# Optimization experiments

Measured on AMD Instinct MI355X. Metric: run time of the kernel, lower is better.

## Reference

```python
import jax, jax.numpy as jnp
import numpy as np

H = 12  # max_heads

def setup_inputs() -> dict:
    key = jax.random.key(0)
    ks = jax.random.split(key, 5)
    B, N, E = 8, 1024, 768
    return {
        "x": jax.random.normal(ks[0], (B, N, E), dtype=jnp.float32),
        "w_qkv": jax.random.normal(ks[1], (3 * E, E), dtype=jnp.float32) * 0.02,
        "b_qkv": jax.random.normal(ks[2], (3 * E,), dtype=jnp.float32) * 0.02,
        "w_proj": jax.random.normal(ks[3], (E, E), dtype=jnp.float32) * 0.02,
        "b_proj": jax.random.normal(ks[4], (E,), dtype=jnp.float32) * 0.02,
        "active_heads": 8,
    }

def reference(x, w_qkv, b_qkv, w_proj, b_proj, active_heads):
    B, N, E = x.shape
    D = E // H
    scale = D ** -0.5
    # qkv projection: [B,N,3E] -> [3,B,H,N,D]
    qkv = (x @ w_qkv.T + b_qkv).reshape(B, N, 3, H, D)
    qkv = jnp.transpose(qkv, (2, 0, 3, 1, 4))
    q, k, v = qkv[0], qkv[1], qkv[2]
    # head mask from active_heads (static int)
    head_mask = (jnp.arange(H) < active_heads).astype(x.dtype)
    m = head_mask[None, :, None, None]
    q = q * m
    k = k * m
    v = v * m
    attn = jax.nn.softmax(jnp.einsum("bhqd,bhkd->bhqk", q, k) * scale, axis=-1)
    out = jnp.einsum("bhqk,bhkd->bhqd", attn, v)
    out = jnp.transpose(out, (0, 2, 1, 3)).reshape(B, N, E)
    channel_mask = jnp.repeat(head_mask, D)  # [E]
    out = out * channel_mask[None, None, :]
    return out @ w_proj.T + b_proj
```

## Files before the change

### kernel.cpp

```cpp
#include <hip/hip_runtime.h>
#include <hip/hip_fp16.h>

#define NH 12
#define BSZ 8
#define NSEQ 1024
#define EDIM 768
#define DH 64

typedef _Float16 f16;
typedef f16 half8 __attribute__((ext_vector_type(8)));
typedef f16 half4 __attribute__((ext_vector_type(4)));
typedef float f32x4 __attribute__((ext_vector_type(4)));
typedef unsigned int u32;
typedef u32 u32x2 __attribute__((ext_vector_type(2)));

static __device__ __forceinline__ void gload16(const void* g, void* l) {
    __builtin_amdgcn_global_load_lds((const __attribute__((address_space(1))) u32*)g,
                                     (__attribute__((address_space(3))) u32*)l, 16, 0, 0);
}
static __device__ __forceinline__ u32 pkrtz(float a, float b) {
    auto h = __builtin_amdgcn_cvt_pkrtz(a, b);
    return __builtin_bit_cast(u32, h);
}
#define MFMA16(a, b, c) __builtin_amdgcn_mfma_f32_16x16x32_f16((a), (b), (c), 0, 0, 0)

__global__ void cvt_all_kernel(const float* __restrict__ x, const float* __restrict__ wq,
                               const float* __restrict__ wp, f16* __restrict__ dst) {
    const int NX = BSZ * NSEQ * EDIM;
    const int NWQ = 3 * EDIM * EDIM;
    int i = (blockIdx.x * blockDim.x + threadIdx.x) * 4;
    const float* s;
    int j;
    if (i < NX) { s = x; j = i; }
    else if (i < NX + NWQ) { s = wq; j = i - NX; }
    else { s = wp; j = i - NX - NWQ; }
    float4 v = *(const float4*)(s + j);
    half4 o = { (f16)v.x, (f16)v.y, (f16)v.z, (f16)v.w };
    *(half4*)(dst + i) = o;
}

template<int MODE>
__global__ __launch_bounds__(256) void gemm_kernel(
    const f16* __restrict__ A, const f16* __restrict__ Wt, const float* __restrict__ bias,
    f16* __restrict__ qbuf, f16* __restrict__ kbuf, f16* __restrict__ vbuf,
    float* __restrict__ outp, const int* __restrict__ activep, int Kd, int NCd)
{
    __shared__ __align__(16) f16 Ah[2][2][4][64][8];
    __shared__ __align__(16) f16 Bh[2][2][4][64][8];

    constexpr int K = EDIM;
    constexpr int NKT = K / 32;
    constexpr int NB = (MODE == 0) ? 18 : 6;

    const int lin = blockIdx.x;
    const int xcd = lin & 7, pos = lin >> 3;
    const int bx = pos % NB;
    const int my = xcd + (pos / NB) * 8;
    const int c0 = bx * 128;
    const int m0 = my * 128;
    const int ah = *activep;
    if (MODE == 0) {
        if (((c0 % EDIM) >> 6) >= ah) return;
    }
    const int nkt = (MODE == 1) ? (2 * ah) : NKT;
    const int tid = threadIdx.x;
    const int lane = tid & 63;
    const int wid  = tid >> 6;
    const int wr = wid >> 1;
    const int wc = wid & 1;
    const int r16 = lane & 15, rg = lane >> 4;

    f32x4 acc[4][4];
#pragma unroll
    for (int i = 0; i < 4; ++i)
#pragma unroll
        for (int j = 0; j < 4; ++j)
            acc[i][j] = f32x4{0.f, 0.f, 0.f, 0.f};

    const int s0 = 2 * wid, s1 = 2 * wid + 1;
    const f16* gA0 = A  + (size_t)(m0 + (s0 >> 2) * 64 + (s0 & 3) * 16 + r16) * K + rg * 8;
    const f16* gA1 = A  + (size_t)(m0 + (s1 >> 2) * 64 + (s1 & 3) * 16 + r16) * K + rg * 8;
    const f16* gB0 = Wt + (size_t)(c0 + (s0 >> 2) * 64 + (s0 & 3) * 16 + r16) * K + rg * 8;
    const f16* gB1 = Wt + (size_t)(c0 + (s1 >> 2) * 64 + (s1 & 3) * 16 + r16) * K + rg * 8;

    auto stage = [&](int buf, int kt) {
        gload16(gA0 + kt * 32, &Ah[buf][s0 >> 2][s0 & 3][0][0]);
        gload16(gA1 + kt * 32, &Ah[buf][s1 >> 2][s1 & 3][0][0]);
        gload16(gB0 + kt * 32, &Bh[buf][s0 >> 2][s0 & 3][0][0]);
        gload16(gB1 + kt * 32, &Bh[buf][s1 >> 2][s1 & 3][0][0]);
    };

    if (nkt > 0) stage(0, 0);
    if (nkt > 1) stage(1, 1);
    asm volatile("s_waitcnt vmcnt(4)" ::: "memory");
    __builtin_amdgcn_s_barrier();
    __builtin_amdgcn_sched_barrier(0);

#pragma unroll 1
    for (int kt = 0; kt < nkt; ++kt) {
        const int cur = kt & 1;
        half8 af[4], bf[4];
#pragma unroll
        for (int f = 0; f < 4; ++f) {
            af[f] = *(const half8*)&Ah[cur][wr][f][lane][0];
            bf[f] = *(const half8*)&Bh[cur][wc][f][lane][0];
        }
        asm volatile("s_waitcnt lgkmcnt(0)" ::: "memory");
        __builtin_amdgcn_sched_barrier(0);
        __builtin_amdgcn_s_barrier();
        __builtin_amdgcn_sched_barrier(0);
        if (kt + 2 < nkt) stage(cur, kt + 2);
        __builtin_amdgcn_sched_barrier(0);
        __builtin_amdgcn_s_setprio(1);
#pragma unroll
        for (int fm = 0; fm < 4; ++fm)
#pragma unroll
            for (int fn = 0; fn < 4; ++fn)
                acc[fm][fn] = MFMA16(af[fm], bf[fn], acc[fm][fn]);
        __builtin_amdgcn_s_setprio(0);
        if (kt + 1 < nkt) {
            if (kt + 2 < nkt) asm volatile("s_waitcnt vmcnt(4)" ::: "memory");
            else              asm volatile("s_waitcnt vmcnt(0)" ::: "memory");
            __builtin_amdgcn_s_barrier();
            __builtin_amdgcn_sched_barrier(0);
        }
    }

#pragma unroll
    for (int fn = 0; fn < 4; ++fn) {
        const int c = c0 + wc * 64 + fn * 16 + r16;
        const float bv = bias[c];
        const bool colActive = (MODE == 1) || (((c % EDIM) >> 6) < ah);
#pragma unroll
        for (int fm = 0; fm < 4; ++fm) {
            const int mbase = m0 + wr * 64 + fm * 16 + rg * 4;
#pragma unroll
            for (int r = 0; r < 4; ++r) {
                const float val = acc[fm][fn][r] + bv;
                const int m = mbase + r;
                if (MODE == 1) {
                    outp[(size_t)m * EDIM + c] = val;
                } else if (colActive) {
                    const int s  = c / EDIM;
                    const int cc = c % EDIM;
                    const int hh = cc >> 6, d = cc & 63;
                    const int bb = m >> 10, n = m & 1023;
                    f16* dst = (s == 0) ? qbuf : ((s == 1) ? kbuf : vbuf);
                    dst[(((size_t)bb * NH + hh) * NSEQ + n) * DH + d] = (f16)val;
                }
            }
        }
    }
}

__global__ __launch_bounds__(256) void vtrans_kernel(const f16* __restrict__ vbuf,
                                                     f16* __restrict__ vtb,
                                                     const int* __restrict__ activep) {
    const int b = blockIdx.z, h = blockIdx.y;
    if (h >= *activep) return;
    const int n0 = blockIdx.x * 64;
    __shared__ __align__(16) f16 T[64][72];
    const f16* src = vbuf + (((size_t)b * NH + h) * NSEQ + n0) * DH;
    f16* dst = vtb + ((size_t)b * NH + h) * DH * NSEQ;
    const int t = threadIdx.x;
    const int rn = t >> 2, rc = t & 3;
    *(half8*)&T[rn][rc * 16]     = *(const half8*)&src[(size_t)rn * DH + rc * 16];
    *(half8*)&T[rn][rc * 16 + 8] = *(const half8*)&src[(size_t)rn * DH + rc * 16 + 8];
    __syncthreads();
    const int d = t >> 2, nc = (t & 3) * 16;
    half8 o0, o1;
#pragma unroll
    for (int j = 0; j < 8; ++j) {
        o0[j] = T[nc + j][d];
        o1[j] = T[nc + 8 + j][d];
    }
    *(half8*)&dst[(size_t)d * NSEQ + n0 + nc]     = o0;
    *(half8*)&dst[(size_t)d * NSEQ + n0 + nc + 8] = o1;
}

__global__ __launch_bounds__(512) void attn_kernel(
    const f16* __restrict__ qbuf, const f16* __restrict__ kbuf, const f16* __restrict__ vtb,
    f16* __restrict__ ctx, const int* __restrict__ activep)
{
    __shared__ __align__(16) f16 Kh[2][2][64][64];
    __shared__ __align__(16) f16 Vh[2][2][64][64];
    __shared__ __align__(16) f16 Ph[8][16][64];

    const int b = blockIdx.z, h = blockIdx.y;
    const int q0 = blockIdx.x * 128;
    const int tid = threadIdx.x, lane = tid & 63, wid = tid >> 6;

    if (h >= *activep) return;

    const size_t hb = (((size_t)b * NH + h) * NSEQ) * DH;
    const f16* Q  = qbuf + hb;
    const char* Kp = (const char*)(kbuf + hb);
    const char* Vp = (const char*)(vtb + hb);

    const int ql = lane & 15;
    const int g  = lane >> 4;
    const int q7 = ql & 7;

    half8 qb0, qb1;
    {
        const f16 qsc = (f16)0.18033688f;
        const f16* qp = Q + (size_t)(q0 + wid * 16 + ql) * DH + g * 8;
        qb0 = *(const half8*)qp        * qsc;
        qb1 = *(const half8*)(qp + 32) * qsc;
    }
    const half8 ones = { (f16)1, (f16)1, (f16)1, (f16)1, (f16)1, (f16)1, (f16)1, (f16)1 };

    const int srow8 = lane >> 3;
    const int schk  = (lane & 7) ^ srow8;
    const int qh4   = wid & 3;

    auto stage = [&](int buf, int pp) {
#pragma unroll
        for (int hf = 0; hf < 2; ++hf) {
            const int kt = 2 * pp + hf;
            if (wid < 4) {
                const char* kb = Kp + (size_t)kt * 8192;
#pragma unroll
                for (int i = 0; i < 2; ++i) {
                    const int r = qh4 * 16 + i * 8 + srow8;
                    gload16(kb + (size_t)r * 128 + schk * 16, &Kh[buf][hf][qh4 * 16 + i * 8][0]);
                }
            } else {
#pragma unroll
                for (int i = 0; i < 2; ++i) {
                    const int r = qh4 * 16 + i * 8 + srow8;
                    gload16(Vp + (size_t)r * (NSEQ * 2) + (size_t)kt * 128 + schk * 16,
                            &Vh[buf][hf][qh4 * 16 + i * 8][0]);
                }
            }
        }
    };

    f32x4 oacc[4];
#pragma unroll
    for (int i = 0; i < 4; ++i) oacc[i] = f32x4{0.f, 0.f, 0.f, 0.f};
    f32x4 lacc = f32x4{0.f, 0.f, 0.f, 0.f};
    float mr = -INFINITY;

    char* prow = (char*)&Ph[wid][ql][0];

    stage(0, 0);
    const int NP = NSEQ / 128;
#pragma unroll 1
    for (int pp = 0; pp < NP; ++pp) {
        const int cur = pp & 1;
        __syncthreads();
        if (pp + 1 < NP) stage(cur ^ 1, pp + 1);

        f32x4 st[2][4];
        __builtin_amdgcn_s_setprio(1);
#pragma unroll
        for (int hf = 0; hf < 2; ++hf)
#pragma unroll
            for (int s = 0; s < 4; ++s) {
                f32x4 t = f32x4{0.f, 0.f, 0.f, 0.f};
                t = MFMA16(*(const half8*)((const char*)&Kh[cur][hf][16 * s + ql][0] + ((g ^ q7) << 4)),       qb0, t);
                t = MFMA16(*(const half8*)((const char*)&Kh[cur][hf][16 * s + ql][0] + (((4 | g) ^ q7) << 4)), qb1, t);
                st[hf][s] = t;
            }
        __builtin_amdgcn_s_setprio(0);

        float pmax;
        {
            float c0 = fmaxf(fmaxf(st[0][0][0], st[0][0][1]), st[0][0][2]);
            float c1 = fmaxf(fmaxf(st[0][0][3], st[0][1][0]), st[0][1][1]);
            float c2 = fmaxf(fmaxf(st[0][1][2], st[0][1][3]), st[0][2][0]);
            float c3 = fmaxf(fmaxf(st[0][2][1], st[0][2][2]), st[0][2][3]);
            float c4 = fmaxf(fmaxf(st[0][3][0], st[0][3][1]), st[0][3][2]);
            float c5 = fmaxf(fmaxf(st[0][3][3], st[1][0][0]), st[1][0][1]);
            float c6 = fmaxf(fmaxf(st[1][0][2], st[1][0][3]), st[1][1][0]);
            float c7 = fmaxf(fmaxf(st[1][1][1], st[1][1][2]), st[1][1][3]);
            float c8 = fmaxf(fmaxf(st[1][2][0], st[1][2][1]), st[1][2][2]);
            float c9 = fmaxf(fmaxf(st[1][2][3], st[1][3][0]), st[1][3][1]);
            float ca = fmaxf(st[1][3][2], st[1][3][3]);
            float d0 = fmaxf(fmaxf(c0, c1), c2);
            float d1 = fmaxf(fmaxf(c3, c4), c5);
            float d2 = fmaxf(fmaxf(c6, c7), c8);
            float d3 = fmaxf(c9, ca);
            pmax = fmaxf(fmaxf(d0, d1), fmaxf(d2, d3));
        }
        pmax = fmaxf(pmax, __shfl_xor(pmax, 16));
        pmax = fmaxf(pmax, __shfl_xor(pmax, 32));

        const float mnew = fmaxf(mr, pmax);
        const float sc = exp2f(mr - mnew);
#pragma unroll
        for (int hf = 0; hf < 2; ++hf)
#pragma unroll
            for (int s = 0; s < 4; ++s)
#pragma unroll
                for (int r = 0; r < 4; ++r)
                    st[hf][s][r] = exp2f(st[hf][s][r] - mnew);
        mr = mnew;

#pragma unroll
        for (int r = 0; r < 4; ++r) {
            const float scr = __shfl(sc, (g << 2) | r);
            oacc[0][r] *= scr; oacc[1][r] *= scr; oacc[2][r] *= scr; oacc[3][r] *= scr;
            lacc[r] *= scr;
        }

#pragma unroll
        for (int hf = 0; hf < 2; ++hf) {
#pragma unroll
            for (int s = 0; s < 4; ++s) {
                u32x2 w = { pkrtz(st[hf][s][0], st[hf][s][1]), pkrtz(st[hf][s][2], st[hf][s][3]) };
                *(u32x2*)(prow + ((32 * s + 8 * g) ^ (q7 << 4))) = w;
            }
            const half8 pa0 = *(const half8*)(prow + ((16 * g) ^ (q7 << 4)));
            const half8 pa1 = *(const half8*)(prow + ((64 + 16 * g) ^ (q7 << 4)));

            __builtin_amdgcn_s_setprio(1);
            lacc = MFMA16(pa0, ones, lacc);
            lacc = MFMA16(pa1, ones, lacc);
#pragma unroll
            for (int db = 0; db < 4; ++db) {
                oacc[db] = MFMA16(pa0, *(const half8*)((const char*)&Vh[cur][hf][16 * db + ql][0] + ((g ^ q7) << 4)),       oacc[db]);
                oacc[db] = MFMA16(pa1, *(const half8*)((const char*)&Vh[cur][hf][16 * db + ql][0] + (((4 | g) ^ q7) << 4)), oacc[db]);
            }
            __builtin_amdgcn_s_setprio(0);
        }
    }

#pragma unroll
    for (int r = 0; r < 4; ++r) {
        const float li = 1.0f / lacc[r];
        const int n = q0 + wid * 16 + (g << 2) + r;
#pragma unroll
        for (int db = 0; db < 4; ++db)
            ctx[((size_t)b * NSEQ + n) * EDIM + h * DH + db * 16 + ql] = (f16)(oacc[db][r] * li);
    }
}

extern "C" void kernel_launch(void* const* d_in, const int* in_sizes, int n_in,
                              void* d_out, int out_size, void* d_ws, size_t ws_size,
                              hipStream_t stream) {
    const float* x      = (const float*)d_in[0];
    const float* w_qkv  = (const float*)d_in[1];
    const float* b_qkv  = (const float*)d_in[2];
    const float* w_proj = (const float*)d_in[3];
    const float* b_proj = (const float*)d_in[4];
    const int*   active = (const int*)d_in[5];
    float* out = (float*)d_out;

    char* ws = (char*)d_ws;
    const size_t n_x  = (size_t)BSZ * NSEQ * EDIM;
    const size_t n_wq = (size_t)3 * EDIM * EDIM;
    const size_t n_wp = (size_t)EDIM * EDIM;
    const size_t n_hd = (size_t)BSZ * NH * NSEQ * DH;

    f16* xh   = (f16*)ws;
    f16* wqh  = xh + n_x;
    f16* wph  = wqh + n_wq;
    f16* qh   = wph + n_wp;
    f16* kh   = qh + n_hd;
    f16* vh   = kh + n_hd;
    f16* ctxh = vh + n_hd;
    f16* vtb  = xh;

    const size_t n_cvt = n_x + n_wq + n_wp;
    cvt_all_kernel<<<(int)(n_cvt / 4 / 256), 256, 0, stream>>>(x, w_qkv, w_proj, xh);

    gemm_kernel<0><<<dim3(64 * 18), 256, 0, stream>>>(
        xh, wqh, b_qkv, qh, kh, vh, nullptr, active, EDIM, 3 * EDIM);

    vtrans_kernel<<<dim3(NSEQ / 64, NH, BSZ), 256, 0, stream>>>(vh, vtb, active);

    attn_kernel<<<dim3(NSEQ / 128, NH, BSZ), 512, 0, stream>>>(qh, kh, vtb, ctxh, active);

    gemm_kernel<1><<<dim3(64 * 6), 256, 0, stream>>>(
        ctxh, wph, b_proj, nullptr, nullptr, nullptr, out, active, EDIM, EDIM);
}
```

Before: 117.5 us.

## Fuse V transpose into QKV GEMM epilogue via shared-memory staging

Removes the separate V-transpose kernel. V-column tiles of the QKV GEMM now stage their outputs in LDS transposed and write them directly as [d][n] rows with 16-byte stores. This saves one kernel launch plus a full write and read of V, at the cost of extra LDS and a sync in the V-tile epilogue. The VT buffer moves to its own workspace slot instead of aliasing x.

```diff
diff --git a/kernel.cpp b/kernel.cpp
--- a/kernel.cpp
+++ b/kernel.cpp
@@ -42,15 +42,17 @@
 template<int MODE>
 __global__ __launch_bounds__(256) void gemm_kernel(
     const f16* __restrict__ A, const f16* __restrict__ Wt, const float* __restrict__ bias,
-    f16* __restrict__ qbuf, f16* __restrict__ kbuf, f16* __restrict__ vbuf,
+    f16* __restrict__ qbuf, f16* __restrict__ kbuf, f16* __restrict__ vtbuf,
     float* __restrict__ outp, const int* __restrict__ activep, int Kd, int NCd)
 {
-    __shared__ __align__(16) f16 Ah[2][2][4][64][8];
-    __shared__ __align__(16) f16 Bh[2][2][4][64][8];
-
     constexpr int K = EDIM;
     constexpr int NKT = K / 32;
     constexpr int NB = (MODE == 0) ? 18 : 6;
+    constexpr int SMSZ = (MODE == 0) ? 34816 : 32768;
+
+    __shared__ __align__(16) char smem[SMSZ];
+    f16 (*Ah)[2][4][64][8] = (f16 (*)[2][4][64][8])smem;
+    f16 (*Bh)[2][4][64][8] = (f16 (*)[2][4][64][8])(smem + 16384);
 
     const int lin = blockIdx.x;
     const int xcd = lin & 7, pos = lin >> 3;
@@ -124,6 +126,36 @@
             __builtin_amdgcn_s_barrier();
             __builtin_amdgcn_sched_barrier(0);
         }
+    }
+
+    if (MODE == 0 && c0 >= 2 * EDIM) {
+        f16 (*T)[136] = (f16 (*)[136])smem;
+        __syncthreads();
+#pragma unroll
+        for (int fn = 0; fn < 4; ++fn) {
+            const int cl = wc * 64 + fn * 16 + r16;
+            const float bv = bias[c0 + cl];
+#pragma unroll
+            for (int fm = 0; fm < 4; ++fm) {
+                const int ml = wr * 64 + fm * 16 + rg * 4;
+                half4 o = { (f16)(acc[fm][fn][0] + bv), (f16)(acc[fm][fn][1] + bv),
+                            (f16)(acc[fm][fn][2] + bv), (f16)(acc[fm][fn][3] + bv) };
+                *(half4*)&T[cl][ml] = o;
+            }
+        }
+        __syncthreads();
+        const int cc0 = c0 - 2 * EDIM;
+        const int bb = m0 >> 10, n0 = m0 & 1023;
+        const int row = tid >> 1, hsel = tid & 1;
+        const int hh = (cc0 + row) >> 6;
+        if (hh < ah) {
+            f16* dst = vtbuf + (((size_t)bb * NH + hh) * DH + ((cc0 + row) & 63)) * NSEQ
+                     + n0 + hsel * 64;
+#pragma unroll
+            for (int j = 0; j < 8; ++j)
+                *(half8*)(dst + j * 8) = *(const half8*)&T[row][hsel * 64 + j * 8];
+        }
+        return;
     }
 
 #pragma unroll
@@ -145,37 +177,12 @@
                     const int cc = c % EDIM;
                     const int hh = cc >> 6, d = cc & 63;
                     const int bb = m >> 10, n = m & 1023;
-                    f16* dst = (s == 0) ? qbuf : ((s == 1) ? kbuf : vbuf);
+                    f16* dst = (s == 0) ? qbuf : kbuf;
                     dst[(((size_t)bb * NH + hh) * NSEQ + n) * DH + d] = (f16)val;
                 }
             }
         }
     }
-}
-
-__global__ __launch_bounds__(256) void vtrans_kernel(const f16* __restrict__ vbuf,
-                                                     f16* __restrict__ vtb,
-                                                     const int* __restrict__ activep) {
-    const int b = blockIdx.z, h = blockIdx.y;
-    if (h >= *activep) return;
-    const int n0 = blockIdx.x * 64;
-    __shared__ __align__(16) f16 T[64][72];
-    const f16* src = vbuf + (((size_t)b * NH + h) * NSEQ + n0) * DH;
-    f16* dst = vtb + ((size_t)b * NH + h) * DH * NSEQ;
-    const int t = threadIdx.x;
-    const int rn = t >> 2, rc = t & 3;
-    *(half8*)&T[rn][rc * 16]     = *(const half8*)&src[(size_t)rn * DH + rc * 16];
-    *(half8*)&T[rn][rc * 16 + 8] = *(const half8*)&src[(size_t)rn * DH + rc * 16 + 8];
-    __syncthreads();
-    const int d = t >> 2, nc = (t & 3) * 16;
-    half8 o0, o1;
-#pragma unroll
-    for (int j = 0; j < 8; ++j) {
-        o0[j] = T[nc + j][d];
-        o1[j] = T[nc + 8 + j][d];
-    }
-    *(half8*)&dst[(size_t)d * NSEQ + n0 + nc]     = o0;
-    *(half8*)&dst[(size_t)d * NSEQ + n0 + nc + 8] = o1;
 }
 
 __global__ __launch_bounds__(512) void attn_kernel(
@@ -359,17 +366,14 @@
     f16* wph  = wqh + n_wq;
     f16* qh   = wph + n_wp;
     f16* kh   = qh + n_hd;
-    f16* vh   = kh + n_hd;
-    f16* ctxh = vh + n_hd;
-    f16* vtb  = xh;
+    f16* vtb  = kh + n_hd;
+    f16* ctxh = vtb + n_hd;
 
     const size_t n_cvt = n_x + n_wq + n_wp;
     cvt_all_kernel<<<(int)(n_cvt / 4 / 256), 256, 0, stream>>>(x, w_qkv, w_proj, xh);
 
     gemm_kernel<0><<<dim3(64 * 18), 256, 0, stream>>>(
-        xh, wqh, b_qkv, qh, kh, vh, nullptr, active, EDIM, 3 * EDIM);
-
-    vtrans_kernel<<<dim3(NSEQ / 64, NH, BSZ), 256, 0, stream>>>(vh, vtb, active);
+        xh, wqh, b_qkv, qh, kh, vtb, nullptr, active, EDIM, 3 * EDIM);
 
     attn_kernel<<<dim3(NSEQ / 128, NH, BSZ), 512, 0, stream>>>(qh, kh, vtb, ctxh, active);
 
```

New measurement: 112.3 us. 4.4% less time.
